# Optimization experiments

Measured on AMD Instinct MI355X. Metric: run time of the kernel, lower is better.

The kernel has to match this reference:

```python
import jax, jax.numpy as jnp
import numpy as np

N, C, K, FF, CO, H = 60000, 128, 32, 512, 128, 8
DH = C // H
EPS = 1e-5
VOXEL_SIZE = np.array([0.1, 0.1, 0.2], dtype=np.float32)
PC_MIN = np.array([-40.0, -40.0, -3.0], dtype=np.float32)


def setup_inputs():
    key = jax.random.key(0)
    ks = jax.random.split(key, 12)
    features = jax.random.normal(ks[0], (N, C), jnp.float32)
    # indices: (N, 4) = [batch_idx, z, y, x]; batch_size = 1
    indices = jax.random.randint(ks[1], (N, 4), 0, 400).astype(jnp.int32)
    indices = indices.at[:, 0].set(0)
    # gathered neighbor indices; negative -> padded (masked); col 0 = self so no row is fully masked
    key_indices = jax.random.randint(ks[2], (N, K), -(N // 3), N).astype(jnp.int32)
    key_indices = key_indices.at[:, 0].set(jnp.arange(N, dtype=jnp.int32))
    w = lambda k, sh: jax.random.normal(k, sh, jnp.float32) * 0.02
    return dict(
        features=features, indices=indices, key_indices=key_indices,
        in_proj_w=w(ks[3], (3 * C, C)), in_proj_b=jnp.zeros((3 * C,), jnp.float32),
        out_w=w(ks[4], (C, C)), out_b=jnp.zeros((C,), jnp.float32),
        qpos_w=w(ks[5], (C, 3)), qpos_b=jnp.zeros((C,), jnp.float32),
        kpos_w=w(ks[6], (C, 3)), kpos_b=jnp.zeros((C,), jnp.float32),
        norm1_g=jnp.ones((C,), jnp.float32), norm1_b=jnp.zeros((C,), jnp.float32),
        norm2_g=jnp.ones((C,), jnp.float32), norm2_b=jnp.zeros((C,), jnp.float32),
        lin1_w=w(ks[7], (FF, C)), lin1_b=jnp.zeros((FF,), jnp.float32),
        lin2_w=w(ks[8], (C, FF)), lin2_b=jnp.zeros((C,), jnp.float32),
        outl_w=w(ks[9], (CO, C)), outl_b=jnp.zeros((CO,), jnp.float32),
        bn_out_g=jnp.ones((CO,), jnp.float32), bn_out_b=jnp.zeros((CO,), jnp.float32),
    )


def batchnorm(x, g, b):
    # BatchNorm1d training-mode forward: batch statistics over voxel dim
    m = jnp.mean(x, axis=0)
    v = jnp.mean((x - m) ** 2, axis=0)
    return (x - m) * jax.lax.rsqrt(v + EPS) * g + b


def reference(features, indices, key_indices, in_proj_w, in_proj_b, out_w, out_b,
              qpos_w, qpos_b, kpos_w, kpos_b, norm1_g, norm1_b, norm2_g, norm2_b,
              lin1_w, lin1_b, lin2_w, lin2_b, outl_w, outl_b, bn_out_g, bn_out_b):
    mask = key_indices < 0                        # (N, K) True = padded key
    gidx = jnp.where(mask, 0, key_indices)        # clamp for safe gather
    # with_coords: voxel centers from [x,y,z] grid indices
    coords = (indices[:, jnp.array([3, 2, 1])].astype(jnp.float32) + 0.5) * jnp.asarray(VOXEL_SIZE) + jnp.asarray(PC_MIN)  # (N,3)
    key_feat = features[gidx]                     # grouping_operation: (N,K,C)
    key_coords = coords[gidx]                     # (N,K,3)
    rel = key_coords - coords[:, None, :]         # use_relative_coords
    # k_pos_proj: 1x1 Conv1d(3->C) + ReLU == pointwise linear over keys
    key_feat = key_feat + jax.nn.relu(jnp.einsum('nkj,cj->nkc', rel, kpos_w) + kpos_b)
    # q_pos_proj: Linear(3->C) + ReLU
    q = features + jax.nn.relu(coords @ qpos_w.T + qpos_b)   # (N,C)
    # MultiheadAttention: seq_len(query)=1, batch=N, seq_len(key)=K
    wq, wk, wv = jnp.split(in_proj_w, 3, axis=0)
    bq, bk, bv = jnp.split(in_proj_b, 3, axis=0)
    qh = (q @ wq.T + bq).reshape(N, H, DH)
    kh = (key_feat @ wk.T + bk).reshape(N, K, H, DH)
    vh = (key_feat @ wv.T + bv).reshape(N, K, H, DH)
    scale = 1.0 / float(np.sqrt(DH))
    scores = jnp.einsum('nhd,nkhd->nhk', qh, kh) * scale      # (N,H,K)
    scores = jnp.where(mask[:, None, :], jnp.finfo(scores.dtype).min, scores)
    attn = jax.nn.softmax(scores, axis=-1)
    att = jnp.einsum('nhk,nkhd->nhd', attn, vh).reshape(N, C) @ out_w.T + out_b
    # residual + BN + FFN + BN + output head
    x = batchnorm(features + att, norm1_g, norm1_b)
    ff = jax.nn.relu(x @ lin1_w.T + lin1_b) @ lin2_w.T + lin2_b
    x = batchnorm(x + ff, norm2_g, norm2_b)
    return jax.nn.relu(batchnorm(x @ outl_w.T + outl_b, bn_out_g, bn_out_b))
```

## Files before the change

kernel.cpp:

```cpp
#include <hip/hip_runtime.h>

#define NPTS 60000
#define C 128
#define K 32
#define FF 512
#define CO 128
#define H 8
#define DH 16
#define EPS 1e-5f

constexpr int OFF_INPROJ_W = 0;
constexpr int OFF_INPROJ_B = 49152;
constexpr int OFF_OUT_W    = 49536;
constexpr int OFF_OUT_B    = 65920;
constexpr int OFF_QPOS_W   = 66048;
constexpr int OFF_QPOS_B   = 66432;
constexpr int OFF_KPOS_W   = 66560;
constexpr int OFF_KPOS_B   = 66944;
constexpr int OFF_N1G      = 67072;
constexpr int OFF_N1B      = 67200;
constexpr int OFF_N2G      = 67328;
constexpr int OFF_N2B      = 67456;
constexpr int OFF_LIN1_W   = 67584;
constexpr int OFF_LIN1_B   = 133120;
constexpr int OFF_LIN2_W   = 133632;
constexpr int OFF_LIN2_B   = 199168;
constexpr int OFF_OUTL_W   = 199296;
constexpr int OFF_OUTL_B   = 215680;
constexpr int OFF_BOG      = 215808;
constexpr int OFF_BOB      = 215936;
constexpr int WTOTAL       = 216064;

constexpr int B_INPROJ = 0;
constexpr int B_OUTW   = 49152;
constexpr int B_LIN1   = 65536;
constexpr int B_LIN2   = 131072;
constexpr int B_OUTL   = 196608;
constexpr int B_WKT    = 212992;
constexpr int B_KPW4   = 229376;
constexpr int B_M      = 230400;
constexpr int B_OB2    = 361472;
constexpr size_t OFF_WB_BYTES  = 1587456;
constexpr size_t OFF_BIG_BYTES = 2310912;
constexpr size_t QK_BYTES = (size_t)NPTS * 1024 * 2;

typedef __attribute__((ext_vector_type(8))) short bfrag8;
typedef __attribute__((ext_vector_type(4))) float f32x4;

__device__ __forceinline__ float bf2f(unsigned short s) {
    return __uint_as_float(((unsigned)s) << 16);
}
__device__ __forceinline__ unsigned short f2bf(float f) {
    unsigned u = __float_as_uint(f);
    u += 0x7fffu + ((u >> 16) & 1u);
    return (unsigned short)(u >> 16);
}
__device__ __forceinline__ float ldE(const float* p, long i) { return p[i]; }
__device__ __forceinline__ float ldE(const unsigned short* p, long i) { return bf2f(p[i]); }
__device__ __forceinline__ void stE(float* p, long i, float v) { p[i] = v; }
__device__ __forceinline__ void stE(unsigned short* p, long i, float v) { p[i] = f2bf(v); }
__device__ __forceinline__ float ldF(const void* p, long i, int bf) {
    return bf ? bf2f(((const unsigned short*)p)[i]) : ((const float*)p)[i];
}
__device__ __forceinline__ bfrag8 ldfrag(const unsigned short* base, int stride, int lane, int k0) {
    return *(const bfrag8*)(base + (lane & 15) * stride + k0 + ((lane >> 4) << 3));
}
__device__ __forceinline__ unsigned cvtpk(float lo, float hi) {
    unsigned r;
    asm("v_cvt_pk_bf16_f32 %0, %1, %2" : "=v"(r) : "v"(lo), "v"(hi));
    return r;
}

__global__ __launch_bounds__(256) void k_detect(const unsigned short* __restrict__ f,
                                                int* __restrict__ flag) {
    __shared__ int cnt_s;
    if (threadIdx.x == 0) cnt_s = 0;
    __syncthreads();
    int sane = 0;
    for (int j = 0; j < 16; ++j) {
        unsigned short u = f[threadIdx.x * 16 + j];
        int e = (u >> 7) & 255;
        sane += (u == 0 || (e >= 100 && e <= 142)) ? 1 : 0;
    }
    atomicAdd(&cnt_s, sane);
    __syncthreads();
    if (threadIdx.x == 0) *flag = (cnt_s >= 3686) ? 1 : 0;
}

struct WTab {
    const void* src[20];
    int beg[20];
    int end[20];
    int bo[20];
};

__global__ __launch_bounds__(256) void k_cvt_weights(WTab tab, float* __restrict__ ws,
                                                     unsigned short* __restrict__ wsB,
                                                     const int* __restrict__ flagp) {
    int bf = *flagp;
    int gid = blockIdx.x * 256 + threadIdx.x;
    #pragma unroll
    for (int j = 0; j < 20; ++j) {
        if (gid >= tab.beg[j] && gid < tab.end[j]) {
            int off = gid - tab.beg[j];
            float v;
            unsigned short raw;
            if (bf) { raw = ((const unsigned short*)tab.src[j])[off]; v = bf2f(raw); }
            else    { v = ((const float*)tab.src[j])[off]; raw = f2bf(v); }
            ws[gid] = v;
            if (tab.bo[j] >= 0) wsB[tab.bo[j] + off] = raw;
            if (j == 0 && off >= 16384 && off < 32768) {
                int r = (off >> 7) - 128;
                int c = off & 127;
                wsB[B_WKT + c * C + r] = raw;
            }
            if (j == 6) {
                int c = off / 3, comp = off - 3 * c;
                ((float*)(wsB + B_KPW4))[c * 4 + comp] = v;
            }
            if (j == 7) {
                ((float*)(wsB + B_KPW4))[off * 4 + 3] = v;
            }
        }
    }
}

__global__ __launch_bounds__(256) void k_mkmat(const float* __restrict__ wsW,
                                               unsigned short* __restrict__ wsBmut) {
    int j = blockIdx.x;
    int t = threadIdx.x;
    const float* outw = wsW + OFF_OUT_W + j * C;
    #pragma unroll
    for (int i = 0; i < 4; ++i) {
        int idx = t + i * 256;
        int h = idx >> 7, cp = idx & 127;
        float s = 0.f;
        const float* wvh = wsW + OFF_INPROJ_W + (256 + h * 16) * C + cp;
        const float* owh = outw + h * 16;
        #pragma unroll
        for (int d = 0; d < 16; ++d)
            s += owh[d] * wvh[d * C];
        int g = j >> 4, c = idx >> 5, r = idx & 31;
        int lane = ((r >> 3) << 4) + (j & 15);
        wsBmut[B_M + (g * 32 + c) * 512 + lane * 8 + (r & 7)] = f2bf(s);
    }
    if (t == 0) {
        float s = wsW[OFF_OUT_B + j];
        const float* bv = wsW + OFF_INPROJ_B + 256;
        for (int c = 0; c < C; ++c) s += outw[c] * bv[c];
        ((float*)(wsBmut + B_OB2))[j] = s;
    }
}

__global__ __launch_bounds__(256) void k_proj(
    const float* __restrict__ wsW, const unsigned short* __restrict__ wsB,
    const void* __restrict__ featv, const int* __restrict__ flagp,
    const int* __restrict__ indices, float* __restrict__ coords,
    unsigned short* __restrict__ Qk)
{
    __shared__ __align__(16) unsigned short sqb[32][136];
    __shared__ __align__(16) unsigned short sqh[32][136];
    __shared__ __align__(16) unsigned short sqk[2][32][136];
    __shared__ float scd[32][4];
    int t = threadIdx.x;
    int row0 = blockIdx.x * 32;
    const int bf = *flagp;
    if (t < 96) {
        int r = t / 3, j = t - 3 * r;
        int n = row0 + r;
        int srci = (j == 0) ? 3 : (j == 1 ? 2 : 1);
        float vs = (j == 2) ? 0.2f : 0.1f;
        float mn = (j == 2) ? -3.0f : -40.0f;
        float v = ((float)indices[n * 4 + srci] + 0.5f) * vs + mn;
        scd[r][j] = v;
        coords[n * 3 + j] = v;
    }
    __syncthreads();
    const float* qpw = wsW + OFF_QPOS_W;
    const float* qpb = wsW + OFF_QPOS_B;
    for (int i = t; i < 32 * C; i += 256) {
        int r = i >> 7, c = i & 127;
        float x = ldF(featv, (long)row0 * C + i, bf);
        float a = qpb[c] + scd[r][0]*qpw[c*3] + scd[r][1]*qpw[c*3+1] + scd[r][2]*qpw[c*3+2];
        sqb[r][c] = f2bf(x + fmaxf(a, 0.0f));
    }
    __syncthreads();
    int lane = t & 63, w = t >> 6;
    int col = lane & 15, quad = lane >> 4;
    for (int tid = w; tid < 16; tid += 4) {
        int mt = tid & 1, nt = tid >> 1, n0 = nt * 16;
        f32x4 acc = {0.f, 0.f, 0.f, 0.f};
        const unsigned short* aB = &sqb[mt*16][0];
        const unsigned short* bB = wsB + B_INPROJ + n0 * C;
        #pragma unroll
        for (int kt = 0; kt < 4; ++kt) {
            bfrag8 a = ldfrag(aB, 136, lane, kt*32);
            bfrag8 b = ldfrag(bB, C, lane, kt*32);
            acc = __builtin_amdgcn_mfma_f32_16x16x32_bf16(a, b, acc, 0, 0, 0);
        }
        #pragma unroll
        for (int r = 0; r < 4; ++r) {
            int n = n0 + col;
            sqh[mt*16 + quad*4 + r][n] = f2bf(acc[r] + wsW[OFF_INPROJ_B + n]);
        }
    }
    __syncthreads();
    const unsigned short* wkT = wsB + B_WKT;
    bfrag8 zf = {0,0,0,0,0,0,0,0};
    for (int h = 0; h < 8; ++h) {
        for (int tid = w; tid < 16; tid += 4) {
            int mt = tid & 1, nt = tid >> 1, n0 = nt * 16;
            bfrag8 a = zf, b = zf;
            if (quad < 2) {
                a = *(const bfrag8*)(&sqh[mt*16 + col][h*16 + quad*8]);
                b = *(const bfrag8*)(wkT + (n0 + col) * C + h*16 + quad*8);
            }
            f32x4 acc = {0.f, 0.f, 0.f, 0.f};
            acc = __builtin_amdgcn_mfma_f32_16x16x32_bf16(a, b, acc, 0, 0, 0);
            #pragma unroll
            for (int r = 0; r < 4; ++r)
                sqk[h & 1][mt*16 + quad*4 + r][n0 + col] = f2bf(acc[r]);
        }
        __syncthreads();
        for (int i = t; i < 2048; i += 256) {
            int r = i >> 6, cp = i & 63;
            unsigned v = *(const unsigned*)&sqk[h & 1][r][2 * cp];
            ((unsigned*)Qk)[(long)(row0 + r) * 512 + h * 64 + cp] = v;
        }
    }
}

__global__ __launch_bounds__(64, 4) void k_attn(
    const float* __restrict__ wsW, const unsigned short* __restrict__ wsB,
    const float* __restrict__ coords, const int* __restrict__ key_idx,
    const void* __restrict__ featv, const int* __restrict__ flagp,
    unsigned short* __restrict__ Qk)
{
    __shared__ __align__(16) unsigned short P[32][136];
    __shared__ __align__(16) float SC[8][36];
    __shared__ __align__(16) float REL[32][4];
    __shared__ __align__(16) int   GS[32];

    int l = threadIdx.x;
    int n = blockIdx.x;
    int col = l & 15, quad = l >> 4;
    int c0 = 2 * l;
    const int bf = *flagp;

    const float* kpwp = wsW + OFF_KPOS_W;
    float kw00 = kpwp[c0*3],   kw01 = kpwp[c0*3+1], kw02 = kpwp[c0*3+2];
    float kw10 = kpwp[c0*3+3], kw11 = kpwp[c0*3+4], kw12 = kpwp[c0*3+5];
    float kb0 = wsW[OFF_KPOS_B + c0], kb1 = wsW[OFF_KPOS_B + c0 + 1];

    if (l < 32) GS[l] = key_idx[n * K + l];
    float cenx = coords[n*3+0], ceny = coords[n*3+1], cenz = coords[n*3+2];
    bfrag8 ak[4];
    {
        const unsigned short* qkrow = Qk + (long)n * 1024 + (col & 7) * 128;
        #pragma unroll
        for (int ks = 0; ks < 4; ++ks)
            ak[ks] = *(const bfrag8*)(qkrow + ks * 32 + quad * 8);
    }
    if (l < 32) {
        int gc = max(GS[l], 0);
        REL[l][0] = coords[gc*3+0] - cenx;
        REL[l][1] = coords[gc*3+1] - ceny;
        REL[l][2] = coords[gc*3+2] - cenz;
        REL[l][3] = 0.f;
    }
    __syncthreads();

    if (bf) {
        const unsigned* xb = (const unsigned*)featv;
        unsigned xv[32];
        #pragma unroll
        for (int k = 0; k < K; ++k) {
            int gcs = __builtin_amdgcn_readfirstlane(max(GS[k], 0));
            xv[k] = xb[(long)gcs * 64 + l];
        }
        #pragma unroll
        for (int k = 0; k < K; ++k) {
            float4 rr = *(const float4*)&REL[k][0];
            float p0 = bf2f((unsigned short)xv[k])
                     + fmaxf(kb0 + rr.x*kw00 + rr.y*kw01 + rr.z*kw02, 0.f);
            float p1 = bf2f((unsigned short)(xv[k] >> 16))
                     + fmaxf(kb1 + rr.x*kw10 + rr.y*kw11 + rr.z*kw12, 0.f);
            *(unsigned*)&P[k][c0] = cvtpk(p0, p1);
        }
    } else {
        const float2* xf = (const float2*)featv;
        #pragma unroll
        for (int kc = 0; kc < K; kc += 16) {
            float2 xv[16];
            #pragma unroll
            for (int j = 0; j < 16; ++j) {
                int gcs = __builtin_amdgcn_readfirstlane(max(GS[kc + j], 0));
                xv[j] = xf[(long)gcs * 64 + l];
            }
            #pragma unroll
            for (int j = 0; j < 16; ++j) {
                int k = kc + j;
                float4 rr = *(const float4*)&REL[k][0];
                float p0 = xv[j].x + fmaxf(kb0 + rr.x*kw00 + rr.y*kw01 + rr.z*kw02, 0.f);
                float p1 = xv[j].y + fmaxf(kb1 + rr.x*kw10 + rr.y*kw11 + rr.z*kw12, 0.f);
                *(unsigned*)&P[k][c0] = cvtpk(p0, p1);
            }
        }
    }
    __syncthreads();

    #pragma unroll
    for (int nt = 0; nt < 2; ++nt) {
        int g = GS[nt * 16 + col];
        f32x4 acc = {0.f, 0.f, 0.f, 0.f};
        #pragma unroll
        for (int ks = 0; ks < 4; ++ks) {
            bfrag8 bp = *(const bfrag8*)(&P[nt * 16 + col][0] + ks * 32 + quad * 8);
            acc = __builtin_amdgcn_mfma_f32_16x16x32_bf16(ak[ks], bp, acc, 0, 0, 0);
        }
        if (quad < 2) {
            #pragma unroll
            for (int r = 0; r < 4; ++r) {
                int h = quad * 4 + r, k = nt * 16 + col;
                SC[h][k] = (g < 0) ? -1e30f : acc[r] * 0.25f;
            }
        }
    }
    __syncthreads();

    {
        int h = l >> 3, sub = l & 7;
        float v0 = SC[h][sub],      v1 = SC[h][sub + 8];
        float v2 = SC[h][sub + 16], v3 = SC[h][sub + 24];
        float m = fmaxf(fmaxf(v0, v1), fmaxf(v2, v3));
        m = fmaxf(m, __shfl_xor(m, 1));
        m = fmaxf(m, __shfl_xor(m, 2));
        m = fmaxf(m, __shfl_xor(m, 4));
        float e0 = __expf(v0 - m), e1 = __expf(v1 - m), e2 = __expf(v2 - m), e3 = __expf(v3 - m);
        float s = e0 + e1 + e2 + e3;
        s += __shfl_xor(s, 1);
        s += __shfl_xor(s, 2);
        s += __shfl_xor(s, 4);
        float inv = 1.0f / s;
        SC[h][sub]      = e0 * inv;
        SC[h][sub + 8]  = e1 * inv;
        SC[h][sub + 16] = e2 * inv;
        SC[h][sub + 24] = e3 * inv;
    }
    __syncthreads();

    {
        union { bfrag8 f; unsigned u32v[4]; } at8;
        #pragma unroll
        for (int j = 0; j < 4; ++j) {
            float a0 = SC[col & 7][quad * 8 + 2*j];
            float a1 = SC[col & 7][quad * 8 + 2*j + 1];
            at8.u32v[j] = cvtpk(a0, a1);
        }
        #pragma unroll
        for (int nt = 0; nt < 8; ++nt) {
            union { bfrag8 f; unsigned short u[8]; } bt;
            #pragma unroll
            for (int j = 0; j < 8; ++j)
                bt.u[j] = P[quad * 8 + j][nt * 16 + col];
            f32x4 d = {0.f, 0.f, 0.f, 0.f};
            d = __builtin_amdgcn_mfma_f32_16x16x32_bf16(at8.f, bt.f, d, 0, 0, 0);
            if (quad < 2) {
                #pragma unroll
                for (int r = 0; r < 4; ++r)
                    P[quad * 4 + r][nt * 16 + col] = f2bf(d[r]);
            }
        }
    }
    __syncthreads();

    {
        unsigned* zout = (unsigned*)(Qk + (long)n * 1024);
        #pragma unroll
        for (int j = 0; j < 8; ++j) {
            int idx = l + j * 64;
            zout[idx] = *(const unsigned*)&P[idx >> 6][(idx & 63) * 2];
        }
    }
}

template <typename T>
__global__ __launch_bounds__(256) void k_outproj(
    const float* __restrict__ wsW, const unsigned short* __restrict__ wsB,
    const void* __restrict__ featv, const int* __restrict__ flagp,
    const unsigned short* __restrict__ Z, T* __restrict__ Y, float* __restrict__ acc_s)
{
    __shared__ float syf[32][132];
    int t = threadIdx.x;
    int row0 = blockIdx.x * 32;
    const int bf = *flagp;
    int lane = t & 63, w = t >> 6;
    int col = lane & 15, quad = lane >> 4;
    const float* ob2 = (const float*)(wsB + B_OB2);
    int mt = w & 1, ntb = w >> 1;
    f32x4 acc[4] = {{0,0,0,0},{0,0,0,0},{0,0,0,0},{0,0,0,0}};
    const unsigned short* zrow = Z + (long)(row0 + mt*16 + col) * 1024 + quad * 8;
    const unsigned short* mbase = wsB + B_M + lane * 8;
    #pragma unroll
    for (int ktc = 0; ktc < 4; ++ktc) {
        bfrag8 a[8];
        #pragma unroll
        for (int j = 0; j < 8; ++j)
            a[j] = *(const bfrag8*)(zrow + (ktc * 8 + j) * 32);
        __builtin_amdgcn_sched_barrier(0);
        bfrag8 bA[8], bB[8];
#define LOADB(dst, ii) { const unsigned short* mb = mbase + ((ntb + 2*(ii))*32 + ktc*8)*512; \
    _Pragma("unroll") for (int j = 0; j < 8; ++j) dst[j] = *(const bfrag8*)(mb + j*512); }
#define MFMA8(buf, ii) { _Pragma("unroll") for (int j = 0; j < 8; ++j) \
    acc[ii] = __builtin_amdgcn_mfma_f32_16x16x32_bf16(a[j], buf[j], acc[ii], 0, 0, 0); }
        LOADB(bA, 0)
        __builtin_amdgcn_sched_barrier(0);
        LOADB(bB, 1)
        __builtin_amdgcn_sched_barrier(0);
        MFMA8(bA, 0)
        LOADB(bA, 2)
        __builtin_amdgcn_sched_barrier(0);
        MFMA8(bB, 1)
        LOADB(bB, 3)
        __builtin_amdgcn_sched_barrier(0);
        MFMA8(bA, 2)
        MFMA8(bB, 3)
#undef LOADB
#undef MFMA8
    }
    #pragma unroll
    for (int i = 0; i < 4; ++i) {
        int n0 = (ntb + 2 * i) * 16;
        #pragma unroll
        for (int r = 0; r < 4; ++r) {
            int m = mt*16 + quad*4 + r;
            int n = n0 + col;
            syf[m][n] = acc[i][r] + ob2[n] + ldF(featv, (long)(row0+m)*C + n, bf);
        }
    }
    __syncthreads();
    for (int i = t; i < 32 * C; i += 256)
        stE(Y, (long)row0 * C + i, syf[i>>7][i&127]);
    if (t < C) {
        float s = 0.f, sq = 0.f;
        for (int r = 0; r < 32; ++r) { float v = syf[r][t]; s += v; sq += v*v; }
        atomicAdd(&acc_s[t], s);
        atomicAdd(&acc_s[C + t], sq);
    }
}

template <typename T>
__global__ __launch_bounds__(256) void k_ffn(
    const float* __restrict__ wsW, const unsigned short* __restrict__ wsB,
    T* __restrict__ Y, const float* __restrict__ acc1, float* __restrict__ acc2)
{
    __shared__ __align__(16) unsigned short sxb[32][136];
    __shared__ __align__(16) unsigned short sh[32][264];
    __shared__ float nsc[C], nsh[C];
    float (*syf)[132] = (float(*)[132])sh;
    int t = threadIdx.x;
    int row0 = blockIdx.x * 32;
    if (t < C) {
        float m = acc1[t] * (1.0f/NPTS);
        float v = acc1[C+t] * (1.0f/NPTS) - m*m;
        float rs = rsqrtf(v + EPS);
        float sc = rs * wsW[OFF_N1G + t];
        nsc[t] = sc;
        nsh[t] = wsW[OFF_N1B + t] - m * sc;
    }
    __syncthreads();
    for (int i = t; i < 32 * C; i += 256) {
        int c = i & 127;
        sxb[i>>7][c] = f2bf(ldE(Y, (long)row0 * C + i) * nsc[c] + nsh[c]);
    }
    __syncthreads();
    int lane = t & 63, w = t >> 6;
    int col = lane & 15, quad = lane >> 4;
    int mtw = w & 1, ntb = w >> 1;
    f32x4 accT[4] = {{0,0,0,0},{0,0,0,0},{0,0,0,0},{0,0,0,0}};
    #pragma unroll
    for (int half = 0; half < 2; ++half) {
        for (int tid = w; tid < 32; tid += 4) {
            int mt = tid & 1, nt = tid >> 1, n0 = nt * 16;
            f32x4 acc = {0.f, 0.f, 0.f, 0.f};
            const unsigned short* aB = &sxb[mt*16][0];
            const unsigned short* bB = wsB + B_LIN1 + (half * 256 + n0) * C;
            bfrag8 bv4[4];
            #pragma unroll
            for (int kt = 0; kt < 4; ++kt)
                bv4[kt] = ldfrag(bB, C, lane, kt*32);
            __builtin_amdgcn_sched_barrier(0);
            #pragma unroll
            for (int kt = 0; kt < 4; ++kt) {
                bfrag8 a = ldfrag(aB, 136, lane, kt*32);
                acc = __builtin_amdgcn_mfma_f32_16x16x32_bf16(a, bv4[kt], acc, 0, 0, 0);
            }
            #pragma unroll
            for (int r = 0; r < 4; ++r) {
                int m = mt*16 + quad*4 + r;
                int nf = half * 256 + n0 + col;
                sh[m][n0 + col] = f2bf(fmaxf(acc[r] + wsW[OFF_LIN1_B + nf], 0.f));
            }
        }
        __syncthreads();
        #pragma unroll
        for (int i = 0; i < 4; ++i) {
            int mt = mtw, n0 = (ntb + 2 * i) * 16;
            const unsigned short* aB = &sh[mt*16][0];
            const unsigned short* bB = wsB + B_LIN2 + (n0 + col) * FF + half * 256;
            bfrag8 b[8];
            #pragma unroll
            for (int kt = 0; kt < 8; ++kt)
                b[kt] = *(const bfrag8*)(bB + kt * 32 + quad * 8);
            __builtin_amdgcn_sched_barrier(0);
            #pragma unroll
            for (int kt = 0; kt < 8; ++kt) {
                bfrag8 a = ldfrag(aB, 264, lane, kt*32);
                accT[i] = __builtin_amdgcn_mfma_f32_16x16x32_bf16(a, b[kt], accT[i], 0, 0, 0);
            }
        }
        __syncthreads();
    }
    #pragma unroll
    for (int i = 0; i < 4; ++i) {
        int n0 = (ntb + 2 * i) * 16;
        #pragma unroll
        for (int r = 0; r < 4; ++r) {
            int m = mtw*16 + quad*4 + r;
            int n = n0 + col;
            syf[m][n] = accT[i][r] + wsW[OFF_LIN2_B + n] + bf2f(sxb[m][n]);
        }
    }
    __syncthreads();
    for (int i = t; i < 32 * C; i += 256)
        stE(Y, (long)row0 * C + i, syf[i>>7][i&127]);
    if (t < C) {
        float s = 0.f, sq = 0.f;
        for (int r = 0; r < 32; ++r) { float v = syf[r][t]; s += v; sq += v*v; }
        atomicAdd(&acc2[t], s);
        atomicAdd(&acc2[C+t], sq);
    }
}

template <typename T>
__global__ __launch_bounds__(256) void k_outl(
    const float* __restrict__ wsW, const unsigned short* __restrict__ wsB,
    T* __restrict__ Y, const float* __restrict__ acc2, float* __restrict__ acc3)
{
    __shared__ __align__(16) unsigned short sxb[32][136];
    __shared__ float syf[32][132];
    __shared__ float nsc[C], nsh[C];
    int t = threadIdx.x;
    int row0 = blockIdx.x * 32;
    if (t < C) {
        float m = acc2[t] * (1.0f/NPTS);
        float v = acc2[C+t] * (1.0f/NPTS) - m*m;
        float rs = rsqrtf(v + EPS);
        float sc = rs * wsW[OFF_N2G + t];
        nsc[t] = sc;
        nsh[t] = wsW[OFF_N2B + t] - m * sc;
    }
    __syncthreads();
    for (int i = t; i < 32 * C; i += 256) {
        int c = i & 127;
        sxb[i>>7][c] = f2bf(ldE(Y, (long)row0 * C + i) * nsc[c] + nsh[c]);
    }
    __syncthreads();
    int lane = t & 63, w = t >> 6;
    int col = lane & 15, quad = lane >> 4;
    for (int tid = w; tid < 16; tid += 4) {
        int mt = tid & 1, nt = tid >> 1, n0 = nt * 16;
        f32x4 acc = {0.f, 0.f, 0.f, 0.f};
        const unsigned short* aB = &sxb[mt*16][0];
        const unsigned short* bB = wsB + B_OUTL + n0 * C;
        bfrag8 bv4[4];
        #pragma unroll
        for (int kt = 0; kt < 4; ++kt)
            bv4[kt] = ldfrag(bB, C, lane, kt*32);
        __builtin_amdgcn_sched_barrier(0);
        #pragma unroll
        for (int kt = 0; kt < 4; ++kt) {
            bfrag8 a = ldfrag(aB, 136, lane, kt*32);
            acc = __builtin_amdgcn_mfma_f32_16x16x32_bf16(a, bv4[kt], acc, 0, 0, 0);
        }
        #pragma unroll
        for (int r = 0; r < 4; ++r) {
            int m = mt*16 + quad*4 + r;
            int n = n0 + col;
            syf[m][n] = acc[r] + wsW[OFF_OUTL_B + n];
        }
    }
    __syncthreads();
    for (int i = t; i < 32 * CO; i += 256)
        stE(Y, (long)row0 * CO + i, syf[i>>7][i&127]);
    if (t < CO) {
        float s = 0.f, sq = 0.f;
        for (int r = 0; r < 32; ++r) { float v = syf[r][t]; s += v; sq += v*v; }
        atomicAdd(&acc3[t], s);
        atomicAdd(&acc3[CO+t], sq);
    }
}

template <typename T>
__global__ __launch_bounds__(256) void k_final(
    const float* __restrict__ wsW, const T* __restrict__ Y,
    const float* __restrict__ acc3, const int* __restrict__ flagp,
    void* __restrict__ out)
{
    long i = (long)blockIdx.x * 256 + threadIdx.x;
    int c = (int)(i & (CO-1));
    float m = acc3[c] * (1.0f/NPTS);
    float v = acc3[CO+c] * (1.0f/NPTS) - m*m;
    float rs = rsqrtf(v + EPS);
    float y = (ldE(Y, i) - m) * rs * wsW[OFF_BOG + c] + wsW[OFF_BOB + c];
    y = fmaxf(y, 0.f);
    if (*flagp) ((unsigned short*)out)[i] = f2bf(y);
    else        ((float*)out)[i] = y;
}

extern "C" void kernel_launch(void* const* d_in, const int* in_sizes, int n_in,
                              void* d_out, int out_size, void* d_ws, size_t ws_size,
                              hipStream_t stream)
{
    char* base = (char*)d_ws;
    float* wsW = (float*)base;
    float* acc1 = wsW + WTOTAL;
    float* acc2 = acc1 + 256;
    float* acc3 = acc2 + 256;
    int* flagp = (int*)(wsW + WTOTAL + 768);
    float* coords = wsW + WTOTAL + 776;
    unsigned short* wsB = (unsigned short*)(base + OFF_WB_BYTES);

    const void* featv = d_in[0];
    const int* indices = (const int*)d_in[1];
    const int* key_idx = (const int*)d_in[2];

    hipMemsetAsync(acc1, 0, 768 * sizeof(float), stream);
    k_detect<<<1, 256, 0, stream>>>((const unsigned short*)d_in[0], flagp);

    static const int cnt[20] = {49152,384,16384,128,384,128,384,128,128,128,
                                128,128,65536,512,65536,128,16384,128,128,128};
    static const int bofs[20] = {B_INPROJ,-1,B_OUTW,-1,-1,-1,-1,-1,-1,-1,
                                 -1,-1,B_LIN1,-1,B_LIN2,-1,B_OUTL,-1,-1,-1};
    WTab tab;
    int off = 0;
    for (int j = 0; j < 20; ++j) {
        tab.src[j] = d_in[3 + j];
        tab.beg[j] = off;
        tab.end[j] = off + cnt[j];
        tab.bo[j] = bofs[j];
        off += cnt[j];
    }
    k_cvt_weights<<<WTOTAL/256, 256, 0, stream>>>(tab, wsW, wsB, flagp);
    k_mkmat<<<128, 256, 0, stream>>>(wsW, wsB);

    size_t bigN = (size_t)NPTS * C;
    bool f32mode = (ws_size >= OFF_BIG_BYTES + QK_BYTES + bigN * 4);

    unsigned short* Qk = (unsigned short*)(base + OFF_BIG_BYTES);

    k_proj<<<NPTS/32, 256, 0, stream>>>(wsW, wsB, featv, flagp, indices, coords, Qk);
    k_attn<<<NPTS, 64, 0, stream>>>(wsW, wsB, coords, key_idx, featv, flagp, Qk);

    if (f32mode) {
        float* Y = (float*)(base + OFF_BIG_BYTES + QK_BYTES);
        k_outproj<float><<<NPTS/32, 256, 0, stream>>>(wsW, wsB, featv, flagp, Qk, Y, acc1);
        k_ffn<float><<<NPTS/32, 256, 0, stream>>>(wsW, wsB, Y, acc1, acc2);
        k_outl<float><<<NPTS/32, 256, 0, stream>>>(wsW, wsB, Y, acc2, acc3);
        k_final<float><<<(NPTS*CO)/256, 256, 0, stream>>>(wsW, Y, acc3, flagp, d_out);
    } else {
        unsigned short* Y = (unsigned short*)(base + OFF_BIG_BYTES + QK_BYTES);
        k_outproj<unsigned short><<<NPTS/32, 256, 0, stream>>>(wsW, wsB, featv, flagp, Qk, Y, acc1);
        k_ffn<unsigned short><<<NPTS/32, 256, 0, stream>>>(wsW, wsB, Y, acc1, acc2);
        k_outl<unsigned short><<<NPTS/32, 256, 0, stream>>>(wsW, wsB, Y, acc2, acc3);
        k_final<unsigned short><<<(NPTS*CO)/256, 256, 0, stream>>>(wsW, Y, acc3, flagp, d_out);
    }
}
```

Before: 610.5 us.

## Split per-point attention work across two wavefronts per block

The attention kernel now launches 128 threads per point instead of 64. Each wavefront gathers and builds half of the 32 key rows, computes one 16-key score tile, and produces half of the P·V output columns. Softmax is spread over 16 lanes per head and the output store is shared between both waves. This halves the serial gather and MFMA chain per wave to expose more memory-level parallelism, at the cost of duplicated Q-fragment and weight loads per wave and more threads per block.

```diff
diff --git a/kernel.cpp b/kernel.cpp
--- a/kernel.cpp
+++ b/kernel.cpp
@@ -230,7 +230,7 @@
     }
 }
 
-__global__ __launch_bounds__(64, 4) void k_attn(
+__global__ __launch_bounds__(128, 8) void k_attn(
     const float* __restrict__ wsW, const unsigned short* __restrict__ wsB,
     const float* __restrict__ coords, const int* __restrict__ key_idx,
     const void* __restrict__ featv, const int* __restrict__ flagp,
@@ -241,7 +241,9 @@
     __shared__ __align__(16) float REL[32][4];
     __shared__ __align__(16) int   GS[32];
 
-    int l = threadIdx.x;
+    int t = threadIdx.x;
+    int l = t & 63;
+    int wv = t >> 6;
     int n = blockIdx.x;
     int col = l & 15, quad = l >> 4;
     int c0 = 2 * l;
@@ -252,8 +254,7 @@
     float kw10 = kpwp[c0*3+3], kw11 = kpwp[c0*3+4], kw12 = kpwp[c0*3+5];
     float kb0 = wsW[OFF_KPOS_B + c0], kb1 = wsW[OFF_KPOS_B + c0 + 1];
 
-    if (l < 32) GS[l] = key_idx[n * K + l];
-    float cenx = coords[n*3+0], ceny = coords[n*3+1], cenz = coords[n*3+2];
+    if (t < 32) GS[t] = key_idx[n * K + t];
     bfrag8 ak[4];
     {
         const unsigned short* qkrow = Qk + (long)n * 1024 + (col & 7) * 128;
@@ -261,45 +262,48 @@
         for (int ks = 0; ks < 4; ++ks)
             ak[ks] = *(const bfrag8*)(qkrow + ks * 32 + quad * 8);
     }
-    if (l < 32) {
-        int gc = max(GS[l], 0);
-        REL[l][0] = coords[gc*3+0] - cenx;
-        REL[l][1] = coords[gc*3+1] - ceny;
-        REL[l][2] = coords[gc*3+2] - cenz;
-        REL[l][3] = 0.f;
-    }
-    __syncthreads();
-
+    if (t < 32) {
+        float cenx = coords[n*3+0], ceny = coords[n*3+1], cenz = coords[n*3+2];
+        int gc = max(GS[t], 0);
+        REL[t][0] = coords[gc*3+0] - cenx;
+        REL[t][1] = coords[gc*3+1] - ceny;
+        REL[t][2] = coords[gc*3+2] - cenz;
+        REL[t][3] = 0.f;
+    }
+    __syncthreads();
+
+    int k0w = wv * 16;
     if (bf) {
         const unsigned* xb = (const unsigned*)featv;
-        unsigned xv[32];
-        #pragma unroll
-        for (int k = 0; k < K; ++k) {
-            int gcs = __builtin_amdgcn_readfirstlane(max(GS[k], 0));
-            xv[k] = xb[(long)gcs * 64 + l];
-        }
-        #pragma unroll
-        for (int k = 0; k < K; ++k) {
+        unsigned xv[16];
+        #pragma unroll
+        for (int j = 0; j < 16; ++j) {
+            int gcs = __builtin_amdgcn_readfirstlane(max(GS[k0w + j], 0));
+            xv[j] = xb[(long)gcs * 64 + l];
+        }
+        #pragma unroll
+        for (int j = 0; j < 16; ++j) {
+            int k = k0w + j;
             float4 rr = *(const float4*)&REL[k][0];
-            float p0 = bf2f((unsigned short)xv[k])
+            float p0 = bf2f((unsigned short)xv[j])
                      + fmaxf(kb0 + rr.x*kw00 + rr.y*kw01 + rr.z*kw02, 0.f);
-            float p1 = bf2f((unsigned short)(xv[k] >> 16))
+            float p1 = bf2f((unsigned short)(xv[j] >> 16))
                      + fmaxf(kb1 + rr.x*kw10 + rr.y*kw11 + rr.z*kw12, 0.f);
             *(unsigned*)&P[k][c0] = cvtpk(p0, p1);
         }
     } else {
         const float2* xf = (const float2*)featv;
         #pragma unroll
-        for (int kc = 0; kc < K; kc += 16) {
-            float2 xv[16];
-            #pragma unroll
-            for (int j = 0; j < 16; ++j) {
-                int gcs = __builtin_amdgcn_readfirstlane(max(GS[kc + j], 0));
+        for (int kc = 0; kc < 16; kc += 8) {
+            float2 xv[8];
+            #pragma unroll
+            for (int j = 0; j < 8; ++j) {
+                int gcs = __builtin_amdgcn_readfirstlane(max(GS[k0w + kc + j], 0));
                 xv[j] = xf[(long)gcs * 64 + l];
             }
             #pragma unroll
-            for (int j = 0; j < 16; ++j) {
-                int k = kc + j;
+            for (int j = 0; j < 8; ++j) {
+                int k = k0w + kc + j;
                 float4 rr = *(const float4*)&REL[k][0];
                 float p0 = xv[j].x + fmaxf(kb0 + rr.x*kw00 + rr.y*kw01 + rr.z*kw02, 0.f);
                 float p1 = xv[j].y + fmaxf(kb1 + rr.x*kw10 + rr.y*kw11 + rr.z*kw12, 0.f);
@@ -309,8 +313,8 @@
     }
     __syncthreads();
 
-    #pragma unroll
-    for (int nt = 0; nt < 2; ++nt) {
+    {
+        int nt = wv;
         int g = GS[nt * 16 + col];
         f32x4 acc = {0.f, 0.f, 0.f, 0.f};
         #pragma unroll
@@ -329,23 +333,22 @@
     __syncthreads();
 
     {
-        int h = l >> 3, sub = l & 7;
-        float v0 = SC[h][sub],      v1 = SC[h][sub + 8];
-        float v2 = SC[h][sub + 16], v3 = SC[h][sub + 24];
-        float m = fmaxf(fmaxf(v0, v1), fmaxf(v2, v3));
+        int h = t >> 4, sub = t & 15;
+        float v0 = SC[h][sub], v1 = SC[h][sub + 16];
+        float m = fmaxf(v0, v1);
         m = fmaxf(m, __shfl_xor(m, 1));
         m = fmaxf(m, __shfl_xor(m, 2));
         m = fmaxf(m, __shfl_xor(m, 4));
-        float e0 = __expf(v0 - m), e1 = __expf(v1 - m), e2 = __expf(v2 - m), e3 = __expf(v3 - m);
-        float s = e0 + e1 + e2 + e3;
+        m = fmaxf(m, __shfl_xor(m, 8));
+        float e0 = __expf(v0 - m), e1 = __expf(v1 - m);
+        float s = e0 + e1;
         s += __shfl_xor(s, 1);
         s += __shfl_xor(s, 2);
         s += __shfl_xor(s, 4);
+        s += __shfl_xor(s, 8);
         float inv = 1.0f / s;
         SC[h][sub]      = e0 * inv;
-        SC[h][sub + 8]  = e1 * inv;
-        SC[h][sub + 16] = e2 * inv;
-        SC[h][sub + 24] = e3 * inv;
+        SC[h][sub + 16] = e1 * inv;
     }
     __syncthreads();
 
@@ -358,7 +361,8 @@
             at8.u32v[j] = cvtpk(a0, a1);
         }
         #pragma unroll
-        for (int nt = 0; nt < 8; ++nt) {
+        for (int i = 0; i < 4; ++i) {
+            int nt = wv * 4 + i;
             union { bfrag8 f; unsigned short u[8]; } bt;
             #pragma unroll
             for (int j = 0; j < 8; ++j)
@@ -377,8 +381,8 @@
     {
         unsigned* zout = (unsigned*)(Qk + (long)n * 1024);
         #pragma unroll
-        for (int j = 0; j < 8; ++j) {
-            int idx = l + j * 64;
+        for (int j = 0; j < 4; ++j) {
+            int idx = t + j * 128;
             zout[idx] = *(const unsigned*)&P[idx >> 6][(idx & 63) * 2];
         }
     }
@@ -660,7 +664,7 @@
     unsigned short* Qk = (unsigned short*)(base + OFF_BIG_BYTES);
 
     k_proj<<<NPTS/32, 256, 0, stream>>>(wsW, wsB, featv, flagp, indices, coords, Qk);
-    k_attn<<<NPTS, 64, 0, stream>>>(wsW, wsB, coords, key_idx, featv, flagp, Qk);
+    k_attn<<<NPTS, 128, 0, stream>>>(wsW, wsB, coords, key_idx, featv, flagp, Qk);
 
     if (f32mode) {
         float* Y = (float*)(base + OFF_BIG_BYTES + QK_BYTES);
```

Result: slower. 648.7 us (+6.3%).
